# Optimization experiments

Measured on AMD Instinct MI355X. Metric: run time of the kernel, lower is better.

## Reference

```python
import jax, jax.numpy as jnp
import numpy as np

N, E, D = 50000, 1600000, 32
P = 2.0  # exponent self.p


def setup_inputs() -> dict:
    key = jax.random.key(0)
    k1, k2, k3 = jax.random.split(key, 3)
    X = jax.random.normal(k1, (N, D), dtype=jnp.float32)
    edge_index = jax.random.randint(k2, (2, E), 0, N)
    W = jax.random.normal(k3, (D, D), dtype=jnp.float32) / np.float32(np.sqrt(D))
    b = jnp.zeros((D,), dtype=jnp.float32)
    return {"X": X, "edge_index": edge_index, "W": W, "b": b}


def gcn_conv(X, edge_index, W, b, n):
    # PyG GCNConv: add self-loops, symmetric deg^-1/2 normalization,
    # aggregate messages from source col -> target row.
    src, dst = edge_index[0], edge_index[1]
    loops = jnp.arange(n)
    row = jnp.concatenate([dst, loops])  # targets
    col = jnp.concatenate([src, loops])  # sources
    deg = jax.ops.segment_sum(jnp.ones(row.shape, X.dtype), row, num_segments=n)
    dinv = jax.lax.rsqrt(jnp.maximum(deg, 1.0))  # deg >= 1 (self-loops)
    h = X @ W  # [N, D]
    msg = h[col] * (dinv[col] * dinv[row])[:, None]  # [E+N, D]
    return jax.ops.segment_sum(msg, row, num_segments=n) + b


def reference(X, edge_index, W, b):
    n = X.shape[0]
    h = jax.nn.relu(gcn_conv(X, edge_index, W, b, n))  # activation(conv(X, ei))
    src, dst = edge_index[0], edge_index[1]
    e = jnp.abs(h[src] - h[dst]) ** P  # [E, D] gather + pow
    s = jax.ops.segment_sum(e, src, num_segments=n)  # scatter-sum by source
    cnt = jax.ops.segment_sum(jnp.ones((e.shape[0],), h.dtype), src, num_segments=n)
    mean = s / jnp.maximum(cnt, 1.0)[:, None]  # scatter-mean finalize
    return jnp.tanh(mean)
```

## Files before the change

kernel.cpp:

```cpp
#include <hip/hip_runtime.h>

#define D 32
#define CSH 7
#define KMASK 127
#define PSH 23
#define PMASK ((1u << PSH) - 1u)
#define NBMAX 512

typedef unsigned int uint;

__device__ inline uint bf16rne(float f) {
    uint u = __float_as_uint(f);
    return (u + 0x7FFFu + ((u >> 16) & 1u)) >> 16;
}
__device__ inline float bf_lo(uint w) { return __uint_as_float(w << 16); }
__device__ inline float bf_hi(uint w) { return __uint_as_float(w & 0xFFFF0000u); }
__device__ inline uint bf_pack(float x, float y) { return bf16rne(x) | (bf16rne(y) << 16); }

__global__ void zero_kernel(int* __restrict__ p, int n) {
    int i = threadIdx.x;
    if (i < n) p[i] = 0;
}

__global__ void coarse_scatter(const int* __restrict__ src, const int* __restrict__ dst,
                               int* __restrict__ gCurD, int* __restrict__ gCurS,
                               uint* __restrict__ coarseD, uint* __restrict__ coarseS,
                               int E, int cap) {
    __shared__ int hD[NBMAX], hS[NBMAX], baseD[NBMAX], baseS[NBMAX];
    int t = threadIdx.x;
    if (t < NBMAX) { hD[t] = 0; hS[t] = 0; }
    __syncthreads();
    int s[4], d[4], lpD[4], lpS[4];
    int j0 = blockIdx.x * 4096 + 4 * t;
    int nv = 0;
    if (j0 + 3 < E) {
        int4 s4 = *(const int4*)(src + j0);
        int4 d4 = *(const int4*)(dst + j0);
        s[0] = s4.x; s[1] = s4.y; s[2] = s4.z; s[3] = s4.w;
        d[0] = d4.x; d[1] = d4.y; d[2] = d4.z; d[3] = d4.w;
        nv = 4;
    } else {
        for (int u = 0; u < 4; ++u) {
            int j = j0 + u;
            if (j < E) { s[nv] = src[j]; d[nv] = dst[j]; ++nv; }
        }
    }
    for (int u = 0; u < nv; ++u) {
        lpD[u] = atomicAdd(&hD[d[u] >> CSH], 1);
        lpS[u] = atomicAdd(&hS[s[u] >> CSH], 1);
    }
    __syncthreads();
    if (t < NBMAX) {
        if (hD[t]) baseD[t] = atomicAdd(&gCurD[t], hD[t]);
        if (hS[t]) baseS[t] = atomicAdd(&gCurS[t], hS[t]);
    }
    __syncthreads();
    for (int u = 0; u < nv; ++u) {
        int bD = d[u] >> CSH, relD = baseD[bD] + lpD[u];
        if (relD < cap)
            coarseD[(size_t)bD * cap + relD] = ((uint)(d[u] & KMASK) << PSH) | (uint)s[u];
        int bS = s[u] >> CSH, relS = baseS[bS] + lpS[u];
        if (relS < cap)
            coarseS[(size_t)bS * cap + relS] = ((uint)(s[u] & KMASK) << PSH) | (uint)d[u];
    }
}

__global__ void deg_dinv_kernel(const uint* __restrict__ coarseD, const int* __restrict__ gCurD,
                                float* __restrict__ dinv, int N, int cap) {
    __shared__ int cnt[128];
    int b = blockIdx.x, t = threadIdx.x;
    if (t < 128) cnt[t] = 0;
    __syncthreads();
    size_t lo = (size_t)b * cap;
    int n = min(gCurD[b], cap - 512);
    int n4 = n >> 2;
    const uint4* c4 = (const uint4*)(coarseD + lo);
    for (int kk = t; kk < n4; kk += 1024) {
        uint4 e4 = c4[kk];
        atomicAdd(&cnt[e4.x >> PSH], 1);
        atomicAdd(&cnt[e4.y >> PSH], 1);
        atomicAdd(&cnt[e4.z >> PSH], 1);
        atomicAdd(&cnt[e4.w >> PSH], 1);
    }
    for (int kk = 4 * n4 + t; kk < n; kk += 1024)
        atomicAdd(&cnt[coarseD[lo + kk] >> PSH], 1);
    __syncthreads();
    int node = (b << CSH) + t;
    if (t < 128 && node < N) dinv[node] = rsqrtf((float)(cnt[t] + 1));
}

__global__ void matmul_scale_kernel(const float* __restrict__ X, const float* __restrict__ W,
                                    const float* __restrict__ dinv, uint* __restrict__ hs16,
                                    int N) {
    __shared__ float Wl[D * D];
    __shared__ float Xl[8 * D];
    int tid = threadIdx.x;
    for (int k = tid; k < D * D; k += 256) Wl[k] = W[k];
    int row0 = blockIdx.x * 8;
    int g = row0 * D + tid;
    Xl[tid] = (g < N * D) ? X[g] : 0.f;
    __syncthreads();
    int r = tid >> 5;
    int d = tid & 31;
    int row = row0 + r;
    float acc = 0.f;
    #pragma unroll
    for (int k = 0; k < D; ++k) acc += Xl[r * D + k] * Wl[k * D + d];
    if (row < N) acc *= dinv[row];
    float other = __shfl_xor(acc, 1);
    if (row < N && (d & 1) == 0)
        hs16[row * 16 + (d >> 1)] = bf_pack(acc, other);
}

__global__ void __launch_bounds__(1024)
conv_fused(const uint* __restrict__ coarseD, const int* __restrict__ gCurD,
           const uint* __restrict__ hs16, const float* __restrict__ bias,
           uint* __restrict__ h2_16, int N, int cap) {
    extern __shared__ uint adjL[];
    __shared__ int cnt[128];
    __shared__ int pre[128];
    __shared__ int rs[128];
    __shared__ int degL[128];
    int b = blockIdx.x;
    int t = threadIdx.x;
    int nodeLo = b << CSH;
    int nNodes = min(128, N - nodeLo);
    if (t < 128) cnt[t] = 0;
    __syncthreads();
    size_t lo = (size_t)b * cap;
    int n = min(gCurD[b], cap - 512);
    int n4 = n >> 2;
    const uint4* c4 = (const uint4*)(coarseD + lo);
    for (int kk = t; kk < n4; kk += 1024) {
        uint4 e4 = c4[kk];
        atomicAdd(&cnt[e4.x >> PSH], 1);
        atomicAdd(&cnt[e4.y >> PSH], 1);
        atomicAdd(&cnt[e4.z >> PSH], 1);
        atomicAdd(&cnt[e4.w >> PSH], 1);
    }
    for (int kk = 4 * n4 + t; kk < n; kk += 1024)
        atomicAdd(&cnt[coarseD[lo + kk] >> PSH], 1);
    __syncthreads();
    int mydeg = 0, mypad = 0;
    if (t < 128) { mydeg = cnt[t]; mypad = (mydeg + 3) & ~3; pre[t] = mypad; }
    __syncthreads();
    for (int off = 1; off < 128; off <<= 1) {
        int x = 0;
        if (t < 128 && t >= off) x = pre[t - off];
        __syncthreads();
        if (t < 128) pre[t] += x;
        __syncthreads();
    }
    if (t < 128) {
        rs[t] = pre[t] - mypad;
        degL[t] = mydeg;
        cnt[t] = pre[t] - mypad;
    }
    __syncthreads();
    for (int kk = t; kk < n; kk += 1024) {
        uint e = coarseD[lo + kk];
        int pos = atomicAdd(&cnt[e >> PSH], 1);
        if (pos < cap) adjL[pos] = e & PMASK;
    }
    __syncthreads();
    int wave = t >> 6, lane = t & 63;
    int p = lane & 15, slot = lane >> 4;
    for (int nl = wave; nl < nNodes; nl += 16) {
        int s = rs[nl];
        int e = s + degL[nl];
        float ax0 = 0.f, ay0 = 0.f, ax1 = 0.f, ay1 = 0.f;
        float ax2 = 0.f, ay2 = 0.f, ax3 = 0.f, ay3 = 0.f;
        int k = s;
        for (; k + 15 < e; k += 16) {
            uint4 iv = *(const uint4*)(adjL + k + slot * 4);
            uint w0 = hs16[iv.x * 16 + p];
            uint w1 = hs16[iv.y * 16 + p];
            uint w2 = hs16[iv.z * 16 + p];
            uint w3 = hs16[iv.w * 16 + p];
            ax0 += bf_lo(w0); ay0 += bf_hi(w0);
            ax1 += bf_lo(w1); ay1 += bf_hi(w1);
            ax2 += bf_lo(w2); ay2 += bf_hi(w2);
            ax3 += bf_lo(w3); ay3 += bf_hi(w3);
        }
        for (; k < e; k += 4) {
            int kk = k + slot;
            if (kk < e) {
                uint w = hs16[adjL[kk] * 16 + p];
                ax0 += bf_lo(w); ay0 += bf_hi(w);
            }
        }
        float accx = (ax0 + ax1) + (ax2 + ax3);
        float accy = (ay0 + ay1) + (ay2 + ay3);
        accx += __shfl_xor(accx, 16); accy += __shfl_xor(accy, 16);
        accx += __shfl_xor(accx, 32); accy += __shfl_xor(accy, 32);
        if (slot == 0) {
            int node = nodeLo + nl;
            uint wself = hs16[(size_t)node * 16 + p];
            float di = rsqrtf((float)(degL[nl] + 1));
            float vx = di * (accx + bf_lo(wself)) + bias[2 * p];
            float vy = di * (accy + bf_hi(wself)) + bias[2 * p + 1];
            h2_16[(size_t)node * 16 + p] = bf_pack(fmaxf(vx, 0.f), fmaxf(vy, 0.f));
        }
    }
}

__global__ void __launch_bounds__(1024)
pow_fused(const uint* __restrict__ coarseS, const int* __restrict__ gCurS,
          const uint* __restrict__ h2_16, float* __restrict__ out, int N, int cap) {
    extern __shared__ uint adjL[];
    __shared__ int cnt[128];
    __shared__ int pre[128];
    __shared__ int rs[128];
    __shared__ int degL[128];
    __shared__ uint self[128 * 16];
    int b = blockIdx.x;
    int t = threadIdx.x;
    int nodeLo = b << CSH;
    int nNodes = min(128, N - nodeLo);
    if (t < 128) cnt[t] = 0;
    for (int i = t; i < nNodes * 16; i += 1024)
        self[i] = h2_16[(size_t)(nodeLo + (i >> 4)) * 16 + (i & 15)];
    __syncthreads();
    size_t lo = (size_t)b * cap;
    int n = min(gCurS[b], cap - 512);
    int n4 = n >> 2;
    const uint4* c4 = (const uint4*)(coarseS + lo);
    for (int kk = t; kk < n4; kk += 1024) {
        uint4 e4 = c4[kk];
        atomicAdd(&cnt[e4.x >> PSH], 1);
        atomicAdd(&cnt[e4.y >> PSH], 1);
        atomicAdd(&cnt[e4.z >> PSH], 1);
        atomicAdd(&cnt[e4.w >> PSH], 1);
    }
    for (int kk = 4 * n4 + t; kk < n; kk += 1024)
        atomicAdd(&cnt[coarseS[lo + kk] >> PSH], 1);
    __syncthreads();
    int mydeg = 0, mypad = 0;
    if (t < 128) { mydeg = cnt[t]; mypad = (mydeg + 3) & ~3; pre[t] = mypad; }
    __syncthreads();
    for (int off = 1; off < 128; off <<= 1) {
        int x = 0;
        if (t < 128 && t >= off) x = pre[t - off];
        __syncthreads();
        if (t < 128) pre[t] += x;
        __syncthreads();
    }
    if (t < 128) {
        rs[t] = pre[t] - mypad;
        degL[t] = mydeg;
        cnt[t] = pre[t] - mypad;
    }
    __syncthreads();
    for (int kk = t; kk < n; kk += 1024) {
        uint e = coarseS[lo + kk];
        int pos = atomicAdd(&cnt[e >> PSH], 1);
        if (pos < cap) adjL[pos] = e & PMASK;
    }
    __syncthreads();
    int wave = t >> 6, lane = t & 63;
    int p = lane & 15, slot = lane >> 4;
    for (int nl = wave; nl < nNodes; nl += 16) {
        int s = rs[nl];
        int e = s + degL[nl];
        uint wh = self[nl * 16 + p];
        float hx = bf_lo(wh), hy = bf_hi(wh);
        float ax0 = 0.f, ay0 = 0.f, ax1 = 0.f, ay1 = 0.f;
        float ax2 = 0.f, ay2 = 0.f, ax3 = 0.f, ay3 = 0.f;
        int k = s;
        for (; k + 15 < e; k += 16) {
            uint4 iv = *(const uint4*)(adjL + k + slot * 4);
            uint w0 = h2_16[iv.x * 16 + p];
            uint w1 = h2_16[iv.y * 16 + p];
            uint w2 = h2_16[iv.z * 16 + p];
            uint w3 = h2_16[iv.w * 16 + p];
            float vx0 = hx - bf_lo(w0), vy0 = hy - bf_hi(w0);
            float vx1 = hx - bf_lo(w1), vy1 = hy - bf_hi(w1);
            float vx2 = hx - bf_lo(w2), vy2 = hy - bf_hi(w2);
            float vx3 = hx - bf_lo(w3), vy3 = hy - bf_hi(w3);
            ax0 += vx0 * vx0; ay0 += vy0 * vy0;
            ax1 += vx1 * vx1; ay1 += vy1 * vy1;
            ax2 += vx2 * vx2; ay2 += vy2 * vy2;
            ax3 += vx3 * vx3; ay3 += vy3 * vy3;
        }
        for (; k < e; k += 4) {
            int kk = k + slot;
            if (kk < e) {
                uint w = h2_16[adjL[kk] * 16 + p];
                float vx = hx - bf_lo(w), vy = hy - bf_hi(w);
                ax0 += vx * vx; ay0 += vy * vy;
            }
        }
        float accx = (ax0 + ax1) + (ax2 + ax3);
        float accy = (ay0 + ay1) + (ay2 + ay3);
        accx += __shfl_xor(accx, 16); accy += __shfl_xor(accy, 16);
        accx += __shfl_xor(accx, 32); accy += __shfl_xor(accy, 32);
        if (slot == 0) {
            float c = fmaxf((float)degL[nl], 1.f);
            float2 r;
            r.x = tanhf(accx / c);
            r.y = tanhf(accy / c);
            ((float2*)out)[(size_t)(nodeLo + nl) * 16 + p] = r;
        }
    }
}

__global__ void fb_count(const int* __restrict__ src, const int* __restrict__ dst,
                         int* __restrict__ degI, int* __restrict__ cntI, int E) {
    int j = blockIdx.x * blockDim.x + threadIdx.x;
    if (j < E) {
        atomicAdd(&degI[dst[j]], 1);
        atomicAdd(&cntI[src[j]], 1);
    }
}
__global__ void fb_dinv(const int* __restrict__ degI, float* __restrict__ dinv, int N) {
    int i = blockIdx.x * blockDim.x + threadIdx.x;
    if (i < N) dinv[i] = rsqrtf((float)(degI[i] + 1));
}
__global__ void fb_matmul(const float* __restrict__ X, const float* __restrict__ W,
                          const float* __restrict__ dinv, float* __restrict__ hs, int N) {
    __shared__ float Wl[D * D];
    __shared__ float Xl[8 * D];
    int tid = threadIdx.x;
    for (int k = tid; k < D * D; k += 256) Wl[k] = W[k];
    int row0 = blockIdx.x * 8;
    int g = row0 * D + tid;
    Xl[tid] = (g < N * D) ? X[g] : 0.f;
    __syncthreads();
    int r = tid >> 5;
    int d = tid & 31;
    int row = row0 + r;
    if (row < N) {
        float acc = 0.f;
        #pragma unroll
        for (int k = 0; k < D; ++k) acc += Xl[r * D + k] * Wl[k * D + d];
        hs[row * D + d] = acc * dinv[row];
    }
}
__global__ void fb_scatter_conv(const int* __restrict__ src, const int* __restrict__ dst,
                                const float* __restrict__ hs, float* __restrict__ S, int ED) {
    int idx = blockIdx.x * blockDim.x + threadIdx.x;
    if (idx < ED) {
        int j = idx >> 5, d = idx & 31;
        atomicAdd(&S[dst[j] * D + d], hs[src[j] * D + d]);
    }
}
__global__ void fb_h2(float* __restrict__ S, const float* __restrict__ hs,
                      const float* __restrict__ dinv, const float* __restrict__ b, int ND) {
    int idx = blockIdx.x * blockDim.x + threadIdx.x;
    if (idx < ND) {
        int i = idx >> 5, d = idx & 31;
        float v = dinv[i] * (S[idx] + hs[idx]) + b[d];
        S[idx] = fmaxf(v, 0.f);
    }
}
__global__ void fb_edge_pow(const int* __restrict__ src, const int* __restrict__ dst,
                            const float* __restrict__ h2, float* __restrict__ out, int ED) {
    int idx = blockIdx.x * blockDim.x + threadIdx.x;
    if (idx < ED) {
        int j = idx >> 5, d = idx & 31;
        float v = h2[src[j] * D + d] - h2[dst[j] * D + d];
        atomicAdd(&out[src[j] * D + d], v * v);
    }
}
__global__ void fb_finalize(float* __restrict__ out, const int* __restrict__ cntI, int ND) {
    int idx = blockIdx.x * blockDim.x + threadIdx.x;
    if (idx < ND) {
        int i = idx >> 5;
        float c = fmaxf((float)cntI[i], 1.f);
        out[idx] = tanhf(out[idx] / c);
    }
}

extern "C" void kernel_launch(void* const* d_in, const int* in_sizes, int n_in,
                              void* d_out, int out_size, void* d_ws, size_t ws_size,
                              hipStream_t stream) {
    const float* X  = (const float*)d_in[0];
    const int*   ei = (const int*)d_in[1];
    const float* W  = (const float*)d_in[2];
    const float* b  = (const float*)d_in[3];
    int N = in_sizes[0] / D;
    int E = in_sizes[1] / 2;
    const int* src = ei;
    const int* dst = ei + E;
    float* out = (float*)d_out;

    size_t ND = (size_t)N * D;
    size_t NH = (size_t)N * 16;
    int nb = (N + 127) >> CSH;
    int cap = ((E + nb - 1) / nb + 1024 + 15) & ~15;
    size_t capSz = (size_t)nb * cap;
    size_t ldsBytes = (size_t)cap * 4;

    uint* coarseD = (uint*)d_ws;
    uint* coarseS = coarseD + capSz;
    uint* hs16   = coarseS + capSz;
    uint* h2_16  = hs16 + NH;
    float* dinv = (float*)(h2_16 + NH);
    int* gCurD  = (int*)(dinv + N);
    int* gCurS  = gCurD + NBMAX;
    size_t need = (2 * capSz + 2 * NH + (size_t)N + 2 * NBMAX) * 4;

    if (ws_size >= need && nb <= NBMAX && N <= (1 << PSH) && capSz < (1u << 30)
        && ldsBytes <= 96 * 1024) {
        zero_kernel<<<1, 1024, 0, stream>>>(gCurD, 2 * NBMAX);
        int cgrid = (E + 4095) / 4096;
        coarse_scatter<<<cgrid, 1024, 0, stream>>>(src, dst, gCurD, gCurS,
                                                   coarseD, coarseS, E, cap);
        deg_dinv_kernel<<<nb, 1024, 0, stream>>>(coarseD, gCurD, dinv, N, cap);
        matmul_scale_kernel<<<(N + 7) / 8, 256, 0, stream>>>(X, W, dinv, hs16, N);
        conv_fused<<<nb, 1024, ldsBytes, stream>>>(coarseD, gCurD, hs16, b, h2_16, N, cap);
        pow_fused<<<nb, 1024, ldsBytes, stream>>>(coarseS, gCurS, h2_16, out, N, cap);
    } else {
        float* fhs  = (float*)d_ws;
        float* S    = fhs + ND;
        float* fdv  = S + ND;
        int*   fdeg = (int*)(fdv + N);
        int*   fcnt = fdeg + N;
        hipMemsetAsync(S, 0, ND * sizeof(float), stream);
        hipMemsetAsync(fdeg, 0, (size_t)2 * N * sizeof(int), stream);
        hipMemsetAsync(d_out, 0, ND * sizeof(float), stream);
        int EDi = E * D, NDi = (int)ND;
        fb_count<<<(E + 255) / 256, 256, 0, stream>>>(src, dst, fdeg, fcnt, E);
        fb_dinv<<<(N + 255) / 256, 256, 0, stream>>>(fdeg, fdv, N);
        fb_matmul<<<(N + 7) / 8, 256, 0, stream>>>(X, W, fdv, fhs, N);
        fb_scatter_conv<<<(EDi + 255) / 256, 256, 0, stream>>>(src, dst, fhs, S, EDi);
        fb_h2<<<(NDi + 255) / 256, 256, 0, stream>>>(S, fhs, fdv, b, NDi);
        fb_edge_pow<<<(EDi + 255) / 256, 256, 0, stream>>>(src, dst, S, out, EDi);
        fb_finalize<<<(NDi + 255) / 256, 256, 0, stream>>>(out, fcnt, NDi);
    }
}
```

Baseline: 98.18 us.

## Stage coarse bucket scatter in shared memory for coalesced global writes

The coarse scatter kernel now computes a block-local prefix sum over bucket histograms, writes each edge into a shared-memory staging buffer sorted by bucket, then copies the staged entries to global memory in contiguous runs per bucket, finding each entry's bucket with a binary search. The goal is to replace the scattered per-edge global stores with mostly consecutive writes. In exchange it adds roughly 40KB of LDS per block, a 9-step scan with barriers, and a binary search per element, which may lower occupancy.

```diff
diff --git a/kernel.cpp b/kernel.cpp
--- a/kernel.cpp
+++ b/kernel.cpp
@@ -22,11 +22,16 @@
     if (i < n) p[i] = 0;
 }
 
-__global__ void coarse_scatter(const int* __restrict__ src, const int* __restrict__ dst,
-                               int* __restrict__ gCurD, int* __restrict__ gCurS,
-                               uint* __restrict__ coarseD, uint* __restrict__ coarseS,
-                               int E, int cap) {
-    __shared__ int hD[NBMAX], hS[NBMAX], baseD[NBMAX], baseS[NBMAX];
+__global__ void __launch_bounds__(1024)
+coarse_scatter(const int* __restrict__ src, const int* __restrict__ dst,
+               int* __restrict__ gCurD, int* __restrict__ gCurS,
+               uint* __restrict__ coarseD, uint* __restrict__ coarseS,
+               int E, int cap) {
+    __shared__ uint stageD[4096], stageS[4096];
+    __shared__ int hD[NBMAX], hS[NBMAX];
+    __shared__ int preD[NBMAX], preS[NBMAX];
+    __shared__ int offD[NBMAX + 1], offS[NBMAX + 1];
+    __shared__ int baseD[NBMAX], baseS[NBMAX];
     int t = threadIdx.x;
     if (t < NBMAX) { hD[t] = 0; hS[t] = 0; }
     __syncthreads();
@@ -50,18 +55,44 @@
         lpS[u] = atomicAdd(&hS[s[u] >> CSH], 1);
     }
     __syncthreads();
-    if (t < NBMAX) {
-        if (hD[t]) baseD[t] = atomicAdd(&gCurD[t], hD[t]);
-        if (hS[t]) baseS[t] = atomicAdd(&gCurS[t], hS[t]);
+    {
+        int l = t & (NBMAX - 1);
+        int* h    = (t < NBMAX) ? hD : hS;
+        int* pre  = (t < NBMAX) ? preD : preS;
+        int* off  = (t < NBMAX) ? offD : offS;
+        int* base = (t < NBMAX) ? baseD : baseS;
+        int* gC   = (t < NBMAX) ? gCurD : gCurS;
+        pre[l] = h[l];
+        __syncthreads();
+        for (int stp = 1; stp < NBMAX; stp <<= 1) {
+            int x = (l >= stp) ? pre[l - stp] : 0;
+            __syncthreads();
+            pre[l] += x;
+            __syncthreads();
+        }
+        off[l] = pre[l] - h[l];
+        if (l == NBMAX - 1) off[NBMAX] = pre[l];
+        if (h[l]) base[l] = atomicAdd(&gC[l], h[l]);
     }
     __syncthreads();
     for (int u = 0; u < nv; ++u) {
-        int bD = d[u] >> CSH, relD = baseD[bD] + lpD[u];
-        if (relD < cap)
-            coarseD[(size_t)bD * cap + relD] = ((uint)(d[u] & KMASK) << PSH) | (uint)s[u];
-        int bS = s[u] >> CSH, relS = baseS[bS] + lpS[u];
-        if (relS < cap)
-            coarseS[(size_t)bS * cap + relS] = ((uint)(s[u] & KMASK) << PSH) | (uint)d[u];
+        stageD[offD[d[u] >> CSH] + lpD[u]] = ((uint)(d[u] & KMASK) << PSH) | (uint)s[u];
+        stageS[offS[s[u] >> CSH] + lpS[u]] = ((uint)(s[u] & KMASK) << PSH) | (uint)d[u];
+    }
+    __syncthreads();
+    int totD = offD[NBMAX];
+    for (int j = t; j < totD; j += 1024) {
+        int lo = 0, hi = NBMAX;
+        while (hi - lo > 1) { int mid = (lo + hi) >> 1; if (offD[mid] <= j) lo = mid; else hi = mid; }
+        int rel = baseD[lo] + (j - offD[lo]);
+        if (rel < cap) coarseD[(size_t)lo * cap + rel] = stageD[j];
+    }
+    int totS = offS[NBMAX];
+    for (int j = t; j < totS; j += 1024) {
+        int lo = 0, hi = NBMAX;
+        while (hi - lo > 1) { int mid = (lo + hi) >> 1; if (offS[mid] <= j) lo = mid; else hi = mid; }
+        int rel = baseS[lo] + (j - offS[lo]);
+        if (rel < cap) coarseS[(size_t)lo * cap + rel] = stageS[j];
     }
 }
 
```

Result: faster. 95.23 us (-3.0%).
